# Performance work log

Measured on AMD Instinct MI355X. Metric: run time of the kernel, lower is better.

The kernel has to match this reference:

```python
import jax, jax.numpy as jnp
import numpy as np

B_, L_, C_ = 4, 2048, 384
EXPAND, H_, N_ = 2, 12, 64
DI = EXPAND * C_          # 768 d_inner
DH = DI // H_             # 64 head dim
HID = 4 * C_              # 1536 mlp hidden
EPS = 1e-5


def layernorm(x, g, b):
    mu = jnp.mean(x, -1, keepdims=True)
    var = jnp.mean((x - mu) ** 2, -1, keepdims=True)
    return (x - mu) * jax.lax.rsqrt(var + EPS) * g + b


def ssm_dir(x, Win, bin_, dtb, Alog, D, Wout, bout):
    """Multihead (Mamba2-style) selective scan. x:(B,L,C) -> (B,L,C)."""
    B, L, _ = x.shape
    zxbcdt = x @ Win + bin_  # (B,L, 2*DI+2*N+H)
    z = zxbcdt[..., :DI]
    xs = zxbcdt[..., DI:2 * DI].reshape(B, L, H_, DH)
    Bt = zxbcdt[..., 2 * DI:2 * DI + N_]
    Ct = zxbcdt[..., 2 * DI + N_:2 * DI + 2 * N_]
    dt = jax.nn.softplus(zxbcdt[..., 2 * DI + 2 * N_:] + dtb)  # (B,L,H)
    A = -jnp.exp(Alog)  # (H,)

    def step(h, inp):
        x_t, B_t, C_t, dt_t = inp  # (B,H,DH),(B,N),(B,N),(B,H)
        a = jnp.exp(dt_t * A)  # (B,H)
        h = a[..., None, None] * h + (dt_t[..., None] * x_t)[..., None] * B_t[:, None, None, :]
        y = jnp.einsum('bhdn,bn->bhd', h, C_t)
        return h, y

    h0 = jnp.zeros((B, H_, DH, N_), x.dtype)
    xsT = jnp.moveaxis(xs, 1, 0)
    _, ys = jax.lax.scan(step, h0, (xsT, jnp.moveaxis(Bt, 1, 0), jnp.moveaxis(Ct, 1, 0), jnp.moveaxis(dt, 1, 0)))
    y = jnp.moveaxis(ys, 0, 1) + D.reshape(H_, DH) * xs  # (B,L,H,DH)
    y = y.reshape(B, L, DI) * jax.nn.silu(z)
    return y @ Wout + bout


def reference(points, g1, be1, g2, be2,
              Winf, binf, dtbf, Alogf, Df, Woutf, boutf,
              Winb, binb, dtbb, Alogb, Db, Woutb, boutb,
              W1, b1m, bng, bnb, W2, b2m):
    # --- token mixer (Parallel bidirectional SSM), pre-norm residual ---
    shortcut = points
    x = layernorm(points, g1, be1)
    fwd = ssm_dir(x, Winf, binf, dtbf, Alogf, Df, Woutf, boutf)
    bwd = jnp.flip(ssm_dir(jnp.flip(x, -2), Winb, binb, dtbb, Alogb, Db, Woutb, boutb), -2)
    x = fwd + bwd + shortcut
    # --- channel mixer (Conv1d k=1 == dense), BatchNorm in eval mode ---
    shortcut = x
    h = layernorm(x, g2, be2)
    h = h @ W1.T + b1m  # (B,L,HID)
    h = (h * (bng / np.sqrt(1.0 + EPS))) + bnb  # BN eval, running mean 0 var 1
    h = jax.nn.relu(h)
    h = h @ W2.T + b2m
    return h + shortcut


def setup_inputs() -> dict:
    key = jax.random.key(0)
    ks = jax.random.split(key, 32)
    s = 0.02
    PROJ = 2 * DI + 2 * N_ + H_

    def dir_params(i):
        return dict(
            Win=jax.random.normal(ks[i], (C_, PROJ)) * s,
            bin_=jnp.zeros((PROJ,)),
            dtb=jnp.log(jnp.expm1(jax.random.uniform(ks[i + 1], (H_,), minval=0.001, maxval=0.1))),
            Alog=jnp.log(jnp.arange(1, H_ + 1, dtype=jnp.float32)),
            D=jnp.ones((DI,)),
            Wout=jax.random.normal(ks[i + 2], (DI, C_)) * s,
            bout=jnp.zeros((C_,)))

    f, b = dir_params(1), dir_params(4)
    return {
        'points': jax.random.normal(ks[0], (B_, L_, C_)),
        'g1': jnp.ones((C_,)), 'be1': jnp.zeros((C_,)),
        'g2': jnp.ones((C_,)), 'be2': jnp.zeros((C_,)),
        'Winf': f['Win'], 'binf': f['bin_'], 'dtbf': f['dtb'], 'Alogf': f['Alog'], 'Df': f['D'], 'Woutf': f['Wout'], 'boutf': f['bout'],
        'Winb': b['Win'], 'binb': b['bin_'], 'dtbb': b['dtb'], 'Alogb': b['Alog'], 'Db': b['D'], 'Woutb': b['Wout'], 'boutb': b['bout'],
        'W1': jax.random.normal(ks[7], (HID, C_)) * s, 'b1m': jnp.zeros((HID,)),
        'bng': jnp.ones((HID,)), 'bnb': jnp.zeros((HID,)),
        'W2': jax.random.normal(ks[8], (C_, HID)) * s, 'b2m': jnp.zeros((C_,)),
    }
```

## Files before the change

kernel.cpp:

```cpp
#include <hip/hip_runtime.h>
#include <hip/hip_bf16.h>

typedef unsigned short u16;
typedef unsigned int   u32;

#define DEVINL static __device__ __forceinline__

constexpr int Bb   = 4;
constexpr int Ll   = 2048;
constexpr int Cc   = 384;
constexpr int Hh   = 12;
constexpr int Nn   = 64;
constexpr int DHh  = 64;
constexpr int DIi  = 768;
constexpr int PROJ = 2*DIi + 2*Nn + Hh;
constexpr int PROJp= 1792;
constexpr int HIDh = 1536;
constexpr int TOK  = Bb*Ll;

constexpr int NWINP  = PROJp*Cc;
constexpr int NWOUTC = Cc*2*DIi;
constexpr int NW1    = HIDh*Cc;
constexpr int NW2    = Cc*HIDh;

typedef __attribute__((ext_vector_type(8))) short bf16x8;
typedef __attribute__((ext_vector_type(4))) float f32x4;

DEVINL float u2f(u32 u){ union { u32 i; float f; } c; c.i = u << 16; return c.f; }
DEVINL u16 f2u(float f){
  u32 x = __float_as_uint(f);
  x += 0x7fffu + ((x >> 16) & 1u);
  return (u16)(x >> 16);
}
DEVINL void ld8f(const u16* p, float* f){
  uint2 w0 = *reinterpret_cast<const uint2*>(p);
  uint2 w1 = *reinterpret_cast<const uint2*>(p + 4);
  f[0]=u2f(w0.x & 0xffffu); f[1]=u2f(w0.x >> 16);
  f[2]=u2f(w0.y & 0xffffu); f[3]=u2f(w0.y >> 16);
  f[4]=u2f(w1.x & 0xffffu); f[5]=u2f(w1.x >> 16);
  f[6]=u2f(w1.y & 0xffffu); f[7]=u2f(w1.y >> 16);
}
DEVINL bf16x8 lds_ld8(const u16* p){
  union { uint2 q[2]; bf16x8 v; } r;
  r.q[0] = *reinterpret_cast<const uint2*>(p);
  r.q[1] = *reinterpret_cast<const uint2*>(p + 4);
  return r.v;
}
DEVINL float ing(const void* p, size_t i, bool f32){
  return f32 ? ((const float*)p)[i] : u2f(((const u16*)p)[i]);
}
DEVINL float softplusf(float v){
  if (v > 20.f) return v;
  return log1pf(expf(v));
}
DEVINL float sigmoidf(float z){
  if (z >= 0.f) { return 1.f / (1.f + expf(-z)); }
  float e = expf(z);
  return e / (1.f + e);
}

DEVINL int xcd_swz2d(){
  int nwg = gridDim.x * gridDim.y;
  int bid = blockIdx.y * gridDim.x + blockIdx.x;
  int qc = nwg >> 3, rc = nwg & 7;
  int xcd = bid & 7, loc = bid >> 3;
  return (xcd < rc) ? (xcd*(qc+1) + loc) : (rc*(qc+1) + (xcd-rc)*qc + loc);
}
DEVINL void xcd_cyb(int& c, int& yy, int& b){
  int ny = gridDim.y, nz = gridDim.z;
  int nwg = gridDim.x * ny * nz;
  int lid = (blockIdx.z*ny + blockIdx.y)*gridDim.x + blockIdx.x;
  int qc = nwg >> 3, rc = nwg & 7;
  int xcd = lid & 7, loc = lid >> 3;
  int swz = (xcd < rc) ? (xcd*(qc+1) + loc) : (rc*(qc+1) + (xcd-rc)*qc + loc);
  yy = swz % ny;
  int t = swz / ny;
  b = t % nz;
  c = t / nz;
}

__global__ void detect_kernel(const u32* __restrict__ g1w, u32* __restrict__ flag){
  if (threadIdx.x == 0 && blockIdx.x == 0)
    flag[0] = (g1w[0] == 0x3F800000u) ? 1u : 0u;
}

__global__ __launch_bounds__(256) void wtr_kernel(
    const void* __restrict__ s0, const void* __restrict__ s1,
    const void* __restrict__ s2, const void* __restrict__ s3,
    u16* __restrict__ wt, const u32* __restrict__ flg)
{
  __shared__ u16 t[32][33];
  bool f32 = flg[0] != 0;
  int z = blockIdx.z;
  const void* src = (z==0)? s0 : (z==1)? s1 : (z==2)? s2 : s3;
  const int R    = (z<2)? Cc   : DIi;
  const int Csrc = (z<2)? PROJ : Cc;
  const int Np   = (z<2)? PROJp: Cc;
  const int dstr = (z<2)? Cc   : 2*DIi;
  const int doff = (z==3)? DIi : 0;
  u16* dst = wt + ((z==0)? 0 : (z==1)? NWINP : 2*NWINP);
  int tilesx = Np/32, tilesy = R/32;
  int tid = blockIdx.x;
  if (tid >= tilesx*tilesy) return;
  int n0 = (tid % tilesx)*32, k0 = (tid / tilesx)*32;
  int tx = threadIdx.x & 31, ty = threadIdx.x >> 5;
  #pragma unroll
  for (int rr=0; rr<32; rr+=8){
    int k = k0+ty+rr, n = n0+tx;
    float v = (n < Csrc) ? ing(src, (size_t)k*Csrc + n, f32) : 0.f;
    t[ty+rr][tx] = f2u(v);
  }
  __syncthreads();
  #pragma unroll
  for (int rr=0; rr<32; rr+=8){
    int n = n0+ty+rr, k = k0+tx;
    dst[(size_t)n*dstr + doff + k] = t[tx][ty+rr];
  }
}

__global__ __launch_bounds__(256) void wcvt2_kernel(
    const void* __restrict__ p0, const void* __restrict__ p1,
    u16* __restrict__ out, const u32* __restrict__ flg)
{
  bool f32 = flg[0] != 0;
  int i = blockIdx.x*256 + threadIdx.x;
  if (i >= NW1 + NW2) return;
  const void* src = (i < NW1) ? p0 : p1;
  int off = (i < NW1) ? i : i - NW1;
  out[i] = f32 ? f2u(((const float*)src)[off]) : ((const u16*)src)[off];
}

template<int MODE>
__global__ __launch_bounds__(256) void ln_kernel(
    const void* __restrict__ in, const void* __restrict__ g,
    const void* __restrict__ be, u16* __restrict__ out, const u32* __restrict__ flg)
{
  bool f32 = flg[0] != 0;
  int tok  = blockIdx.x*4 + (threadIdx.x >> 6);
  int lane = threadIdx.x & 63;
  size_t base = (size_t)tok * Cc;
  float v[6];
  #pragma unroll
  for (int j=0;j<6;j++){
    size_t idx = base + lane + 64*j;
    v[j] = (MODE == 1) ? ((const float*)in)[idx] : ing(in, idx, f32);
  }
  float s = 0.f;
  #pragma unroll
  for (int j=0;j<6;j++) s += v[j];
  #pragma unroll
  for (int o=32;o;o>>=1) s += __shfl_xor(s, o, 64);
  float mu = s * (1.0f/Cc);
  float q = 0.f;
  #pragma unroll
  for (int j=0;j<6;j++){ float d = v[j]-mu; q = fmaf(d,d,q); }
  #pragma unroll
  for (int o=32;o;o>>=1) q += __shfl_xor(q, o, 64);
  float rs = rsqrtf(q*(1.0f/Cc) + 1e-5f);
  #pragma unroll
  for (int j=0;j<6;j++){
    int c = lane + 64*j;
    out[base + c] = f2u((v[j]-mu)*rs*ing(g, c, f32) + ing(be, c, f32));
  }
}

template<int EPI, int BM, int BN>
__global__ __launch_bounds__(256) void mgemm_kernel(
    const u16* __restrict__ A, const u16* __restrict__ A2, int KA,
    const u16* __restrict__ Bm,
    int M, int N, int K, int lda,
    const void* __restrict__ bias, const void* __restrict__ bng,
    const void* __restrict__ bnb,  const void* __restrict__ resb, size_t res_off,
    const float* resf, u16* __restrict__ outb, float* outf, void* outv,
    const u32* __restrict__ flg)
{
  constexpr int WR = (BM == 128) ? 2 : 4;
  constexpr int WC = 4 / WR;
  constexpr int RH = BM / WR;
  constexpr int CW = BN / WC;
  constexpr int SM = RH / 16;
  constexpr int SN = CW / 16;

  bool f32 = flg[0] != 0;
  __shared__ u16 As[BM][36];
  __shared__ u16 Bs[BN][36];
  const int tid  = threadIdx.x;
  const int lane = tid & 63;
  const int w    = tid >> 6;
  const int q    = lane >> 4;
  const int r16  = lane & 15;
  const int wr   = (WC == 1) ? w : (w >> 1);
  const int wc   = (WC == 1) ? 0 : (w & 1);
  const int swz = xcd_swz2d();
  const int m0 = (swz / gridDim.x) * BM, n0 = (swz % gridDim.x) * BN;

  f32x4 acc[SM][SN] = {};

  const int sa_m = tid >> 2, sa_k = (tid & 3) * 8;

  for (int k0 = 0; k0 < K; k0 += 32) {
    const u16* Ab = A; int kc0 = k0;
    if (KA && k0 >= KA){ Ab = A2; kc0 = k0 - KA; }
    #pragma unroll
    for (int p = 0; p < BM/64; p++) {
      int rrow = p*64 + sa_m;
      uint4 v = *reinterpret_cast<const uint4*>(Ab + (size_t)(m0+rrow)*lda + kc0 + sa_k);
      *reinterpret_cast<uint2*>(&As[rrow][sa_k])   = make_uint2(v.x, v.y);
      *reinterpret_cast<uint2*>(&As[rrow][sa_k+4]) = make_uint2(v.z, v.w);
    }
    #pragma unroll
    for (int p = 0; p < BN/64; p++) {
      int n = p*64 + (tid >> 2), kc = (tid & 3) * 8;
      uint4 v = *reinterpret_cast<const uint4*>(Bm + (size_t)(n0+n)*K + k0 + kc);
      *reinterpret_cast<uint2*>(&Bs[n][kc])   = make_uint2(v.x, v.y);
      *reinterpret_cast<uint2*>(&Bs[n][kc+4]) = make_uint2(v.z, v.w);
    }
    __syncthreads();
    bf16x8 af[SM], bfr[SN];
    #pragma unroll
    for (int i=0;i<SM;i++)
      af[i] = lds_ld8(&As[wr*RH + i*16 + r16][q*8]);
    #pragma unroll
    for (int s=0;s<SN;s++)
      bfr[s] = lds_ld8(&Bs[wc*CW + s*16 + r16][q*8]);
    #pragma unroll
    for (int i=0;i<SM;i++)
      #pragma unroll
      for (int s=0;s<SN;s++)
        acc[i][s] = __builtin_amdgcn_mfma_f32_16x16x32_bf16(af[i], bfr[s], acc[i][s], 0,0,0);
    __syncthreads();
  }

  const float RSQ = 0.9999950000374997f;
  #pragma unroll
  for (int i=0;i<SM;i++){
    #pragma unroll
    for (int s=0;s<SN;s++){
      int gcol = n0 + wc*CW + s*16 + r16;
      if (gcol >= N) continue;
      #pragma unroll
      for (int rr=0;rr<4;rr++){
        int grow = m0 + wr*RH + i*16 + q*4 + rr;
        size_t o = (size_t)grow*N + gcol;
        float v = acc[i][s][rr];
        if constexpr (EPI == 0) {
          outb[o] = f2u(v + ing(bias, gcol, f32));
        } else if constexpr (EPI == 1) {
          outf[o] = v + ing(bias, gcol, f32) + ing(bng, gcol, f32)
                      + ing(resb, res_off + o, f32);
        } else if constexpr (EPI == 2) {
          float t = (v + ing(bias, gcol, f32)) * (ing(bng, gcol, f32) * RSQ) + ing(bnb, gcol, f32);
          outb[o] = f2u(t > 0.f ? t : 0.f);
        } else {
          float t = v + ing(bias, gcol, f32) + resf[o];
          if (f32) ((float*)outv)[o] = t; else ((u16*)outv)[o] = f2u(t);
        }
      }
    }
  }
}


__global__ __launch_bounds__(256) void scan_state_kernel(
    const u16* __restrict__ zx, const void* __restrict__ dtb,
    const void* __restrict__ Alog, u16* __restrict__ states,
    float* __restrict__ P, int dir, int QQ, const u32* __restrict__ flg)
{
  bool f32 = flg[0] != 0;
  int c, h, b;
  xcd_cyb(c, h, b);
  int NC = gridDim.x;
  int lane = threadIdx.x & 63;
  int d0   = (threadIdx.x >> 6) * 16;
  float hst[16];
  #pragma unroll
  for (int j=0;j<16;j++) hst[j] = 0.f;
  float Af = -expf(ing(Alog, h, f32));
  float dtbh = ing(dtb, h, f32);
  float p = 1.f;
  for (int i=0;i<QQ;i++){
    int tl = c*QQ + i;
    int t  = dir ? (Ll-1-tl) : tl;
    size_t row = ((size_t)b*Ll + t) * PROJ;
    float dt = softplusf(u2f(zx[row + 2*DIi + 2*Nn + h]) + dtbh);
    float a  = expf(fmaxf(dt*Af, -80.f));
    float u  = dt * u2f(zx[row + 2*DIi + lane]);
    const u16* xrow = zx + row + DIi + h*DHh + d0;
    #pragma unroll
    for (int j=0;j<16;j++) hst[j] = a*hst[j] + u*u2f(xrow[j]);
    p *= a;
  }
  int g = (b*Hh + h)*NC + c;
  u16* sp = states + (size_t)g*4096;
  #pragma unroll
  for (int j=0;j<16;j++) sp[(d0+j)*64 + lane] = f2u(hst[j]);
  if (threadIdx.x == 0) P[g] = p;
}

__global__ __launch_bounds__(256) void scan_state32m4_kernel(
    const u16* __restrict__ zx, const void* __restrict__ dtb,
    const void* __restrict__ Alog, u16* __restrict__ states,
    float* __restrict__ P, int dir, const u32* __restrict__ flg)
{
  constexpr int Q = 32;
  __shared__ u16 Braw[Q][68];
  __shared__ u16 XT[4][64][36];
  __shared__ u16 BwT[4][64][36];
  __shared__ float wv4[4][Q];
  bool f32 = flg[0] != 0;
  int c, hg, b;
  xcd_cyb(c, hg, b);
  int NC = gridDim.x;
  int tid = threadIdx.x;
  int w = tid >> 6, lane = tid & 63;
  int h = hg*4 + w;
  int q = lane >> 4, r16 = lane & 15;
  int g = (b*Hh + h)*NC + c;
  float Af = -expf(ing(Alog, h, f32));
  float dtbh = ing(dtb, h, f32);

  {
    int i = tid >> 3, p = tid & 7;
    int tl = c*Q + i;
    int t  = dir ? (Ll-1-tl) : tl;
    const u16* sb = zx + ((size_t)b*Ll + t)*PROJ + 2*DIi + p*8;
    uint2 b0 = *reinterpret_cast<const uint2*>(sb);
    uint2 b1 = *reinterpret_cast<const uint2*>(sb + 4);
    *reinterpret_cast<uint2*>(&Braw[i][p*8])   = b0;
    *reinterpret_cast<uint2*>(&Braw[i][p*8+4]) = b1;
  }
  #pragma unroll
  for (int rep=0; rep<4; rep++){
    int j = rep*64 + lane;
    int i = j >> 3, p = j & 7;
    int tl = c*Q + i;
    int t  = dir ? (Ll-1-tl) : tl;
    const u16* sx = zx + ((size_t)b*Ll + t)*PROJ + DIi + h*DHh + p*8;
    uint2 a0 = *reinterpret_cast<const uint2*>(sx);
    uint2 a1 = *reinterpret_cast<const uint2*>(sx + 4);
    u16 tmp[8];
    *reinterpret_cast<uint2*>(&tmp[0]) = a0;
    *reinterpret_cast<uint2*>(&tmp[4]) = a1;
    #pragma unroll
    for (int e=0;e<8;e++) XT[w][p*8+e][i] = tmp[e];
  }
  float dt, la;
  {
    int tl = c*Q + (lane & 31);
    int t  = dir ? (Ll-1-tl) : tl;
    float draw = u2f(zx[((size_t)b*Ll + t)*PROJ + 2*DIi + 2*Nn + h]);
    dt = softplusf(draw + dtbh);
    la = fmaxf(dt*Af, -80.f);
  }
  float L = la;
  #pragma unroll
  for (int off=1; off<32; off<<=1){
    float tv = __shfl_up(L, off, 32);
    if ((lane & 31) >= off) L += tv;
  }
  float Lt = __shfl(L, 31, 32);
  if (lane < Q) wv4[w][lane] = expf(fmaxf(Lt - L, -80.f)) * dt;
  if (lane == 0) P[g] = expf(fmaxf(Lt, -87.f));
  __syncthreads();
  #pragma unroll
  for (int rep=0; rep<4; rep++){
    int j = rep*64 + lane;
    int i = j >> 3, p = j & 7;
    float wsc = wv4[w][i];
    u16 tmp[8];
    *reinterpret_cast<uint2*>(&tmp[0]) = *reinterpret_cast<const uint2*>(&Braw[i][p*8]);
    *reinterpret_cast<uint2*>(&tmp[4]) = *reinterpret_cast<const uint2*>(&Braw[i][p*8+4]);
    #pragma unroll
    for (int e=0;e<8;e++) BwT[w][p*8+e][i] = f2u(wsc * u2f(tmp[e]));
  }
  __syncthreads();

  f32x4 acc[4][4] = {};
  bf16x8 af[4];
  #pragma unroll
  for (int mt=0;mt<4;mt++) af[mt] = lds_ld8(&XT[w][mt*16+r16][q*8]);
  #pragma unroll
  for (int nt=0;nt<4;nt++){
    bf16x8 bf = lds_ld8(&BwT[w][nt*16+r16][q*8]);
    #pragma unroll
    for (int mt=0;mt<4;mt++)
      acc[mt][nt] = __builtin_amdgcn_mfma_f32_16x16x32_bf16(af[mt], bf, acc[mt][nt], 0,0,0);
  }
  u16* sp = states + (size_t)g*4096;
  #pragma unroll
  for (int mt=0;mt<4;mt++)
    #pragma unroll
    for (int nt=0;nt<4;nt++)
      #pragma unroll
      for (int rr=0;rr<4;rr++){
        int d = mt*16 + q*4 + rr, n = nt*16 + r16;
        sp[d*64 + n] = f2u(acc[mt][nt][rr]);
      }
}

template<int NC>
__global__ __launch_bounds__(256) void scan_combine_kernel(
    u16* __restrict__ states, const float* __restrict__ P)
{
  __shared__ float ps[(NC > 64) ? NC : 64];
  int g   = blockIdx.x >> 4;
  int idx = ((blockIdx.x & 15) << 8) | threadIdx.x;
  if (threadIdx.x < NC) ps[threadIdx.x] = P[g*NC + threadIdx.x];
  __syncthreads();
  size_t base = (size_t)g*NC*4096 + idx;
  float sv[NC];
  #pragma unroll
  for (int c=0;c<NC;c++) sv[c] = u2f(states[base + (size_t)c*4096]);
  float hr = 0.f;
  #pragma unroll
  for (int c=0;c<NC;c++){
    states[base + (size_t)c*4096] = f2u(hr);
    hr = ps[c]*hr + sv[c];
  }
}

__global__ __launch_bounds__(64) void scan_out_kernel(
    const u16* __restrict__ zx, const void* __restrict__ dtb,
    const void* __restrict__ Alog, const void* __restrict__ Dp,
    const u16* __restrict__ hinit, u16* __restrict__ ych, int dir, int QQ,
    const u32* __restrict__ flg)
{
  bool f32 = flg[0] != 0;
  int c, h, b;
  xcd_cyb(c, h, b);
  int NC = gridDim.x;
  int lane = threadIdx.x;
  int g = (b*Hh + h)*NC + c;
  float hs[64];
  const u16* hp = hinit + (size_t)g*4096 + lane*64;
  #pragma unroll
  for (int n=0;n<64;n++) hs[n] = u2f(hp[n]);
  float Af = -expf(ing(Alog, h, f32));
  float dtbh = ing(dtb, h, f32);
  float Dv = ing(Dp, h*DHh + lane, f32);
  for (int i=0;i<QQ;i++){
    int tl = c*QQ + i;
    int t  = dir ? (Ll-1-tl) : tl;
    size_t row = ((size_t)b*Ll + t) * PROJ;
    float dt = softplusf(u2f(zx[row + 2*DIi + 2*Nn + h]) + dtbh);
    float a  = expf(fmaxf(dt*Af, -80.f));
    float xv = u2f(zx[row + DIi + h*DHh + lane]);
    float zv = u2f(zx[row + h*DHh + lane]);
    const u16* Brow = zx + row + 2*DIi;
    const u16* Crow = Brow + Nn;
    float u = dt * xv;
    float y0=0.f, y1=0.f, y2=0.f, y3=0.f;
    #pragma unroll
    for (int j=0;j<16;j++){
      float h0 = a*hs[j]    + u*u2f(Brow[j]);    hs[j]   =h0; y0 = fmaf(h0, u2f(Crow[j]),    y0);
      float h1 = a*hs[j+16] + u*u2f(Brow[j+16]); hs[j+16]=h1; y1 = fmaf(h1, u2f(Crow[j+16]), y1);
      float h2 = a*hs[j+32] + u*u2f(Brow[j+32]); hs[j+32]=h2; y2 = fmaf(h2, u2f(Crow[j+32]), y2);
      float h3 = a*hs[j+48] + u*u2f(Brow[j+48]); hs[j+48]=h3; y3 = fmaf(h3, u2f(Crow[j+48]), y3);
    }
    float y = (y0+y1)+(y2+y3);
    float yo = y + Dv*xv;
    float sg = zv * sigmoidf(zv);
    ych[((size_t)(b*Ll + t))*DIi + h*DHh + lane] = f2u(yo * sg);
  }
}

__global__ __launch_bounds__(256) void scan_out32m4_kernel(
    const u16* __restrict__ zx, const void* __restrict__ dtb,
    const void* __restrict__ Alog, const void* __restrict__ Dp,
    const u16* __restrict__ hinit, u16* __restrict__ ych, int dir,
    const u32* __restrict__ flg)
{
  constexpr int Q = 32;
  __shared__ u16 bc[Q][132];
  __shared__ u16 XT[4][64][36];
  __shared__ u16 gp[4][Q][36];
  __shared__ float Lss[4][Q], dts[4][Q];
  bool f32 = flg[0] != 0;
  int c, hg, b;
  xcd_cyb(c, hg, b);
  int NC = gridDim.x;
  int tid = threadIdx.x;
  int w = tid >> 6, lane = tid & 63;
  int h = hg*4 + w;
  int q = lane >> 4, r16 = lane & 15;
  int g = (b*Hh + h)*NC + c;
  float Af = -expf(ing(Alog, h, f32));
  float dtbh = ing(dtb, h, f32);

  #pragma unroll
  for (int rep=0; rep<2; rep++){
    int j = rep*256 + tid;
    int i = j >> 4, p = j & 15;
    int tl = c*Q + i;
    int t  = dir ? (Ll-1-tl) : tl;
    const u16* sb = zx + ((size_t)b*Ll + t)*PROJ + 2*DIi + p*8;
    uint2 b0 = *reinterpret_cast<const uint2*>(sb);
    uint2 b1 = *reinterpret_cast<const uint2*>(sb + 4);
    *reinterpret_cast<uint2*>(&bc[i][p*8])   = b0;
    *reinterpret_cast<uint2*>(&bc[i][p*8+4]) = b1;
  }
  #pragma unroll
  for (int rep=0; rep<4; rep++){
    int j = rep*64 + lane;
    int i = j >> 3, p = j & 7;
    int tl = c*Q + i;
    int t  = dir ? (Ll-1-tl) : tl;
    const u16* sx = zx + ((size_t)b*Ll + t)*PROJ + DIi + h*DHh + p*8;
    uint2 a0 = *reinterpret_cast<const uint2*>(sx);
    uint2 a1 = *reinterpret_cast<const uint2*>(sx + 4);
    u16 tmp[8];
    *reinterpret_cast<uint2*>(&tmp[0]) = a0;
    *reinterpret_cast<uint2*>(&tmp[4]) = a1;
    #pragma unroll
    for (int e=0;e<8;e++) XT[w][p*8+e][i] = tmp[e];
  }
  float dt, la;
  {
    int tl = c*Q + (lane & 31);
    int t  = dir ? (Ll-1-tl) : tl;
    float draw = u2f(zx[((size_t)b*Ll + t)*PROJ + 2*DIi + 2*Nn + h]);
    dt = softplusf(draw + dtbh);
    la = fmaxf(dt*Af, -80.f);
  }
  float L = la;
  #pragma unroll
  for (int off=1; off<32; off<<=1){
    float tv = __shfl_up(L, off, 32);
    if ((lane & 31) >= off) L += tv;
  }
  if (lane < Q){ Lss[w][lane] = L; dts[w][lane] = dt; }
  __syncthreads();

  f32x4 gacc[2][2] = {};
  #pragma unroll
  for (int kk=0; kk<2; kk++){
    bf16x8 ac[2], bb[2];
    #pragma unroll
    for (int mt=0;mt<2;mt++) ac[mt] = lds_ld8(&bc[mt*16+r16][64 + kk*32 + q*8]);
    #pragma unroll
    for (int nt=0;nt<2;nt++) bb[nt] = lds_ld8(&bc[nt*16+r16][kk*32 + q*8]);
    #pragma unroll
    for (int mt=0;mt<2;mt++)
      #pragma unroll
      for (int nt=0;nt<2;nt++)
        gacc[mt][nt] = __builtin_amdgcn_mfma_f32_16x16x32_bf16(ac[mt], bb[nt], gacc[mt][nt], 0,0,0);
  }
  float iL[2][4], sL[2], sdt[2];
  #pragma unroll
  for (int mt=0;mt<2;mt++)
    #pragma unroll
    for (int rr=0;rr<4;rr++) iL[mt][rr] = Lss[w][mt*16 + q*4 + rr];
  #pragma unroll
  for (int nt=0;nt<2;nt++){ int s = nt*16 + r16; sL[nt] = Lss[w][s]; sdt[nt] = dts[w][s]; }
  #pragma unroll
  for (int mt=0;mt<2;mt++)
    #pragma unroll
    for (int nt=0;nt<2;nt++)
      #pragma unroll
      for (int rr=0;rr<4;rr++){
        int i = mt*16 + q*4 + rr, s = nt*16 + r16;
        float m = (i >= s) ? expf(fmaxf(iL[mt][rr]-sL[nt], -80.f))*sdt[nt] : 0.f;
        gp[w][i][s] = f2u(gacc[mt][nt][rr] * m);
      }
  __syncthreads();

  f32x4 aI[2][4] = {}, aS[2][4] = {};
  {
    bf16x8 ag[2];
    #pragma unroll
    for (int mt=0;mt<2;mt++) ag[mt] = lds_ld8(&gp[w][mt*16+r16][q*8]);
    #pragma unroll
    for (int nt=0;nt<4;nt++){
      bf16x8 bx = lds_ld8(&XT[w][nt*16+r16][q*8]);
      #pragma unroll
      for (int mt=0;mt<2;mt++)
        aI[mt][nt] = __builtin_amdgcn_mfma_f32_16x16x32_bf16(ag[mt], bx, aI[mt][nt], 0,0,0);
    }
  }
  #pragma unroll
  for (int kk=0; kk<2; kk++){
    bf16x8 ac[2];
    #pragma unroll
    for (int mt=0;mt<2;mt++) ac[mt] = lds_ld8(&bc[mt*16+r16][64 + kk*32 + q*8]);
    #pragma unroll
    for (int nt=0;nt<4;nt++){
      const u16* hp = hinit + (size_t)g*4096 + (nt*16+r16)*64 + kk*32 + q*8;
      bf16x8 bh = *reinterpret_cast<const bf16x8*>(hp);
      #pragma unroll
      for (int mt=0;mt<2;mt++)
        aS[mt][nt] = __builtin_amdgcn_mfma_f32_16x16x32_bf16(ac[mt], bh, aS[mt][nt], 0,0,0);
    }
  }

  float Dv[4];
  #pragma unroll
  for (int nt=0;nt<4;nt++) Dv[nt] = ing(Dp, h*DHh + nt*16 + r16, f32);
  #pragma unroll
  for (int mt=0;mt<2;mt++)
    #pragma unroll
    for (int rr=0;rr<4;rr++){
      int i = mt*16 + q*4 + rr;
      float ei = expf(fmaxf(iL[mt][rr], -87.f));
      int tl = c*Q + i;
      int t  = dir ? (Ll-1-tl) : tl;
      size_t rowz = ((size_t)b*Ll + t)*PROJ + (size_t)h*DHh;
      size_t obase = ((size_t)(b*Ll + t))*DIi + h*DHh;
      #pragma unroll
      for (int nt=0;nt<4;nt++){
        int d = nt*16 + r16;
        float xv = u2f(XT[w][d][i]);
        float zv = u2f(zx[rowz + d]);
        float y  = aI[mt][nt][rr] + ei*aS[mt][nt][rr] + Dv[nt]*xv;
        ych[obase + d] = f2u(y * zv * sigmoidf(zv));
      }
    }
}

extern "C" void kernel_launch(void* const* d_in, const int* in_sizes, int n_in,
                              void* d_out, int out_size, void* d_ws, size_t ws_size,
                              hipStream_t stream)
{
  (void)in_sizes; (void)n_in; (void)out_size;
  const void* points = d_in[0];
  const void* g1   = d_in[1];
  const void* be1  = d_in[2];
  const void* g2   = d_in[3];
  const void* be2  = d_in[4];
  const void* Win[2]  = { d_in[5],  d_in[12] };
  const void* bin[2]  = { d_in[6],  d_in[13] };
  const void* dtb[2]  = { d_in[7],  d_in[14] };
  const void* Alog[2] = { d_in[8],  d_in[15] };
  const void* Dd[2]   = { d_in[9],  d_in[16] };
  const void* Wout[2] = { d_in[10], d_in[17] };
  const void* bout[2] = { d_in[11], d_in[18] };
  const void* W1   = d_in[19];
  const void* b1m  = d_in[20];
  const void* bng  = d_in[21];
  const void* bnb  = d_in[22];
  const void* W2   = d_in[23];
  const void* b2m  = d_in[24];

  auto align256 = [](size_t x){ return (x + 255) & ~(size_t)255; };
  constexpr size_t ZXB  = (size_t)TOK*PROJ*2;
  constexpr size_t YCHB = (size_t)TOK*DIi*2;
  constexpr size_t MLPB = (size_t)TOK*HIDh*2;
  constexpr size_t XB   = (size_t)TOK*Cc*2;
  constexpr size_t X1B  = (size_t)TOK*Cc*4;
  constexpr size_t WTB  = ((size_t)2*NWINP + NWOUTC + NW1 + NW2) * 2;

  auto scan_bytes = [&](int NCc)->size_t {
    size_t STBc = (size_t)Bb*Hh*NCc*4096*2;
    size_t PBc  = align256((size_t)Bb*Hh*NCc*4);
    return ZXB + 2*YCHB + STBc + PBc + 4096;
  };
  auto need_for = [&](int NCc)->size_t {
    size_t scan = scan_bytes(NCc);
    size_t RBc  = scan > MLPB ? scan : MLPB;
    return 256 + align256(XB) + align256(RBc) + align256(X1B) + align256(WTB) + 4096;
  };
  int NCr = 8;
  if (need_for(16) <= ws_size) NCr = 16;
  if (need_for(32) <= ws_size) NCr = 32;
  if (need_for(64) <= ws_size) NCr = 64;
  const int QQr = Ll / NCr;
  const size_t STB = (size_t)Bb*Hh*NCr*4096*2;
  const size_t SCAN = scan_bytes(NCr);
  const size_t RB = SCAN > MLPB ? SCAN : MLPB;

  char* ws = (char*)d_ws;
  size_t off = 0;
  auto alloc = [&](size_t bytes) -> char* {
    char* p = ws + off;
    off += align256(bytes);
    return p;
  };
  u32*   flag = (u32*)  alloc(256);
  u16*   x    = (u16*)  alloc(XB);
  char*  Rbig =         alloc(RB);
  float* x1   = (float*)alloc(X1B);
  u16*   wt   = (u16*)  alloc(WTB);
  u16*   zx     = (u16*)Rbig;
  u16*   ych0   = (u16*)(Rbig + ZXB);
  u16*   ych1   = (u16*)(Rbig + ZXB + YCHB);
  u16*   states = (u16*)(Rbig + ZXB + 2*YCHB);
  float* P      = (float*)(Rbig + ZXB + 2*YCHB + STB);
  u16*   hin2   = x;
  u16*   hmid   = (u16*)Rbig;
  u16* WinT[2]  = { wt, wt + NWINP };
  u16* WoutTT   = wt + 2*NWINP;
  u16* W1b      = wt + 2*NWINP + NWOUTC;
  u16* W2b      = W1b + NW1;
  u16* ychd[2]  = { ych0, ych1 };

  detect_kernel<<<1, 64, 0, stream>>>((const u32*)g1, flag);

  wtr_kernel<<<dim3(672,1,4), 256, 0, stream>>>(
      Win[0], Win[1], Wout[0], Wout[1], wt, flag);
  wcvt2_kernel<<<(NW1+NW2+255)/256, 256, 0, stream>>>(W1, W2, W1b, flag);

  ln_kernel<0><<<TOK/4, 256, 0, stream>>>(points, g1, be1, x, flag);

  for (int dir = 0; dir < 2; dir++) {
    mgemm_kernel<0,128,128><<<dim3(PROJp/128, TOK/128), 256, 0, stream>>>(
        x, nullptr, 0, WinT[dir], TOK, PROJ, Cc, Cc, bin[dir],
        nullptr, nullptr, nullptr, 0, nullptr, zx, nullptr, nullptr, flag);
    if (QQr == 32) {
      scan_state32m4_kernel<<<dim3(NCr, Hh/4, Bb), 256, 0, stream>>>(
          zx, dtb[dir], Alog[dir], states, P, dir, flag);
    } else {
      scan_state_kernel<<<dim3(NCr,Hh,Bb), 256, 0, stream>>>(
          zx, dtb[dir], Alog[dir], states, P, dir, QQr, flag);
    }
    if (NCr == 64)      scan_combine_kernel<64><<<Bb*Hh*16, 256, 0, stream>>>(states, P);
    else if (NCr == 32) scan_combine_kernel<32><<<Bb*Hh*16, 256, 0, stream>>>(states, P);
    else if (NCr == 16) scan_combine_kernel<16><<<Bb*Hh*16, 256, 0, stream>>>(states, P);
    else                scan_combine_kernel< 8><<<Bb*Hh*16, 256, 0, stream>>>(states, P);
    if (QQr == 32) {
      scan_out32m4_kernel<<<dim3(NCr, Hh/4, Bb), 256, 0, stream>>>(
          zx, dtb[dir], Alog[dir], Dd[dir], states, ychd[dir], dir, flag);
    } else {
      scan_out_kernel<<<dim3(NCr,Hh,Bb), 64, 0, stream>>>(
          zx, dtb[dir], Alog[dir], Dd[dir], states, ychd[dir], dir, QQr, flag);
    }
  }

  mgemm_kernel<1,64,64><<<dim3(Cc/64, TOK/64), 256, 0, stream>>>(
      ych0, ych1, DIi, WoutTT, TOK, Cc, 2*DIi, DIi, bout[0],
      bout[1], nullptr, points, 0, nullptr,
      nullptr, x1, nullptr, flag);

  ln_kernel<1><<<TOK/4, 256, 0, stream>>>(x1, g2, be2, hin2, flag);

  mgemm_kernel<2,128,128><<<dim3(HIDh/128, TOK/128), 256, 0, stream>>>(
      hin2, nullptr, 0, W1b, TOK, HIDh, Cc, Cc, b1m,
      bng, bnb, nullptr, 0, nullptr, hmid, nullptr, nullptr, flag);

  mgemm_kernel<3,64,64><<<dim3(Cc/64, TOK/64), 256, 0, stream>>>(
      hmid, nullptr, 0, W2b, TOK, Cc, HIDh, HIDh, b2m,
      nullptr, nullptr, nullptr, 0, x1, nullptr, nullptr, d_out, flag);
}
```

Measured before the change: 404.0 us.

## Use direct global-to-LDS loads with XOR-swizzled tiles and BK=64 in GEMM

The GEMM staging loop now issues global_load_lds 16-byte direct copies into shared memory instead of going through registers. The shared tiles drop the padded layout for an XOR-swizzled one, and the K step doubles to 64 with two MFMA sub-steps per barrier. This is meant to cut VGPR traffic, LDS store instructions and barrier count per K element. In exchange it doubles LDS use per block, and the swizzle must match the lane-to-address mapping of the direct-load instruction to stay correct.

Result: faster. 373.1 us (-7.6%).

```diff
diff --git a/kernel.cpp b/kernel.cpp
--- a/kernel.cpp
+++ b/kernel.cpp
@@ -57,6 +57,12 @@
   if (z >= 0.f) { return 1.f / (1.f + expf(-z)); }
   float e = expf(z);
   return e / (1.f + e);
+}
+
+DEVINL void gload16(const u16* g, u16* l){
+  __builtin_amdgcn_global_load_lds(
+      (const __attribute__((address_space(1))) void*)g,
+      (__attribute__((address_space(3))) void*)l, 16, 0, 0);
 }
 
 DEVINL int xcd_swz2d(){
@@ -174,6 +180,7 @@
     const float* resf, u16* __restrict__ outb, float* outf, void* outv,
     const u32* __restrict__ flg)
 {
+  constexpr int BK = 64;
   constexpr int WR = (BM == 128) ? 2 : 4;
   constexpr int WC = 4 / WR;
   constexpr int RH = BM / WR;
@@ -182,8 +189,8 @@
   constexpr int SN = CW / 16;
 
   bool f32 = flg[0] != 0;
-  __shared__ u16 As[BM][36];
-  __shared__ u16 Bs[BN][36];
+  __shared__ u16 As[BM*BK] __attribute__((aligned(16)));
+  __shared__ u16 Bs[BN*BK] __attribute__((aligned(16)));
   const int tid  = threadIdx.x;
   const int lane = tid & 63;
   const int w    = tid >> 6;
@@ -196,38 +203,46 @@
 
   f32x4 acc[SM][SN] = {};
 
-  const int sa_m = tid >> 2, sa_k = (tid & 3) * 8;
-
-  for (int k0 = 0; k0 < K; k0 += 32) {
+  const int srow = lane >> 3;
+  const int sgl  = lane & 7;
+
+  for (int k0 = 0; k0 < K; k0 += BK) {
     const u16* Ab = A; int kc0 = k0;
     if (KA && k0 >= KA){ Ab = A2; kc0 = k0 - KA; }
     #pragma unroll
-    for (int p = 0; p < BM/64; p++) {
-      int rrow = p*64 + sa_m;
-      uint4 v = *reinterpret_cast<const uint4*>(Ab + (size_t)(m0+rrow)*lda + kc0 + sa_k);
-      *reinterpret_cast<uint2*>(&As[rrow][sa_k])   = make_uint2(v.x, v.y);
-      *reinterpret_cast<uint2*>(&As[rrow][sa_k+4]) = make_uint2(v.z, v.w);
-    }
-    #pragma unroll
-    for (int p = 0; p < BN/64; p++) {
-      int n = p*64 + (tid >> 2), kc = (tid & 3) * 8;
-      uint4 v = *reinterpret_cast<const uint4*>(Bm + (size_t)(n0+n)*K + k0 + kc);
-      *reinterpret_cast<uint2*>(&Bs[n][kc])   = make_uint2(v.x, v.y);
-      *reinterpret_cast<uint2*>(&Bs[n][kc+4]) = make_uint2(v.z, v.w);
+    for (int j = 0; j < BM/32; j++){
+      int r0  = (w*(BM/32) + j)*8;
+      int row = r0 + srow;
+      int gl  = sgl ^ (row & 7);
+      gload16(Ab + (size_t)(m0+row)*lda + kc0 + gl*8, &As[r0*BK]);
+    }
+    #pragma unroll
+    for (int j = 0; j < BN/32; j++){
+      int r0  = (w*(BN/32) + j)*8;
+      int row = r0 + srow;
+      int gl  = sgl ^ (row & 7);
+      gload16(Bm + (size_t)(n0+row)*K + k0 + gl*8, &Bs[r0*BK]);
     }
     __syncthreads();
-    bf16x8 af[SM], bfr[SN];
-    #pragma unroll
-    for (int i=0;i<SM;i++)
-      af[i] = lds_ld8(&As[wr*RH + i*16 + r16][q*8]);
-    #pragma unroll
-    for (int s=0;s<SN;s++)
-      bfr[s] = lds_ld8(&Bs[wc*CW + s*16 + r16][q*8]);
-    #pragma unroll
-    for (int i=0;i<SM;i++)
-      #pragma unroll
-      for (int s=0;s<SN;s++)
-        acc[i][s] = __builtin_amdgcn_mfma_f32_16x16x32_bf16(af[i], bfr[s], acc[i][s], 0,0,0);
+    #pragma unroll
+    for (int kk = 0; kk < 2; kk++){
+      bf16x8 af[SM], bfr[SN];
+      #pragma unroll
+      for (int i=0;i<SM;i++){
+        int ar = wr*RH + i*16 + r16;
+        af[i] = *reinterpret_cast<const bf16x8*>(&As[ar*BK + (((kk*4+q) ^ (ar&7)) << 3)]);
+      }
+      #pragma unroll
+      for (int s=0;s<SN;s++){
+        int br = wc*CW + s*16 + r16;
+        bfr[s] = *reinterpret_cast<const bf16x8*>(&Bs[br*BK + (((kk*4+q) ^ (br&7)) << 3)]);
+      }
+      #pragma unroll
+      for (int i=0;i<SM;i++)
+        #pragma unroll
+        for (int s=0;s<SN;s++)
+          acc[i][s] = __builtin_amdgcn_mfma_f32_16x16x32_bf16(af[i], bfr[s], acc[i][s], 0,0,0);
+    }
     __syncthreads();
   }
 
```
